# Kernel optimization log

Hardware: AMD Instinct MI355X
Metric: run time of the kernel (lower is better)

## Reference

```python
import jax, jax.numpy as jnp
import numpy as np

LAM = 0.5          # lambda_ in DyGCN
GROUPS = 4
EPS_GN = 1e-5
EPS_LN = 1e-5


def _group_norm(y, w, b):
    # y: [B, Ch, N, T]; GroupNorm over (channels-in-group, N, T)
    B, Ch, N, T = y.shape
    yr = y.reshape(B, GROUPS, Ch // GROUPS, N, T)
    mu = yr.mean(axis=(2, 3, 4), keepdims=True)
    var = yr.var(axis=(2, 3, 4), keepdims=True)
    yn = ((yr - mu) * jax.lax.rsqrt(var + EPS_GN)).reshape(B, Ch, N, T)
    return yn * w[None, :, None, None] + b[None, :, None, None]


def _gtu(X, w, b, pw, pb, qw, qb):
    # grouped conv2d, kernel (1,k), stride 1, VALID; out channels = 2*H
    xc = jax.lax.conv_general_dilated(
        X, w, window_strides=(1, 1), padding='VALID',
        feature_group_count=GROUPS,
        dimension_numbers=('NCHW', 'OIHW', 'NCHW'))
    xc = xc + b[None, :, None, None]
    H = X.shape[1]
    xp = _group_norm(xc[:, :H], pw, pb)   # matches torch chunk(2, dim=1)
    xq = _group_norm(xc[:, H:], qw, qb)
    mish = xp * jnp.tanh(jax.nn.softplus(xp))   # Mish
    gate = jnp.clip(xq, 0.0, 1.0)               # Hardtanh(0,1)
    return mish * gate


def reference(x, static_adj, U1, U2, U3, be, Ve, W0, b0, masks, Ws, bs, Wd, bd,
              conv3_w, conv5_w, conv7_w, conv9_w, conv_b,
              gn_pw, gn_pb, gn_qw, gn_qb, fc_w, fc_b, res_w, res_b, ln_w, ln_b):
    B, N, C, T = x.shape
    # ---- Temporal attention ----
    lhs = jnp.einsum('btc,cn->btn', jnp.einsum('bnct,n->btc', x, U1), U2)  # [B,T,N]
    rhs = jnp.einsum('c,bnct->bnt', U3, x)                                 # [B,N,T]
    product = jnp.einsum('btn,bns->bts', lhs, rhs)                          # [B,T,T]
    E = jnp.einsum('ij,bjk->bik', Ve, jax.nn.sigmoid(product + be))
    At = jax.nn.softmax(E, axis=1)
    x_TAt = jnp.einsum('bmt,bts->bms', x.reshape(B, N * C, T), At).reshape(B, N, C, T)
    # ---- DyGCN, vectorized across T ----
    xt = jnp.moveaxis(x_TAt, -1, 1)                                        # [B,T,N,C]
    x0 = jnp.einsum('btnc,hc->btnh', xt, W0) + b0                          # shared linear
    enh = static_adj[None] * jax.nn.sigmoid(masks)                         # [T,N,N]
    s = jnp.einsum('tnm,btmc->btnc', enh, xt)
    static_out = jnp.einsum('btnc,thc->btnh', s, Ws) + bs[None, :, None, :]
    # dynamic branch (DynamicGCNLayer): data-dependent adjacency
    scores = jnp.einsum('btnc,btmc->btnm', xt, xt) / jnp.sqrt(jnp.float32(C))
    adj = jax.nn.softmax(scores, axis=-1)                                  # [B,T,N,N]
    d = jnp.einsum('btnm,btmc->btnc', adj, xt)
    dyn_out = jnp.einsum('btnc,thc->btnh', d, Wd) + bd[None, :, None, :]
    fused = (LAM - 0.025) * static_out + (1.0 - LAM - 0.025) * dyn_out + 0.05 * x0
    X = jnp.transpose(fused, (0, 3, 2, 1))                                 # [B,H,N,T]
    # ---- multi-scale gated temporal convs ----
    outs = [
        _gtu(X, conv3_w, conv_b[0], gn_pw[0], gn_pb[0], gn_qw[0], gn_qb[0]),
        _gtu(X, conv5_w, conv_b[1], gn_pw[1], gn_pb[1], gn_qw[1], gn_qb[1]),
        _gtu(X, conv7_w, conv_b[2], gn_pw[2], gn_pb[2], gn_qw[2], gn_qb[2]),
        _gtu(X, conv9_w, conv_b[3], gn_pw[3], gn_pb[3], gn_qw[3], gn_qb[3]),
    ]
    tc = jnp.concatenate(outs, axis=-1)                                    # [B,H,N,4T-20]
    tc = jnp.einsum('bhnk,ok->bhno', tc, fc_w) + fc_b                      # fcmy (dropout=eval no-op)
    tco = jax.nn.relu(tc)                                                  # [B,H,N,T]
    # ---- residual + LayerNorm ----
    residual = jnp.einsum('bnct,hc->bhnt', x, res_w) + res_b[None, :, None, None]
    y = jax.nn.relu(residual + tco)                                        # [B,H,N,T]
    yp = jnp.transpose(y, (0, 3, 2, 1))                                    # [B,T,N,H]
    mu = yp.mean(axis=-1, keepdims=True)
    var = yp.var(axis=-1, keepdims=True)
    yn = (yp - mu) * jax.lax.rsqrt(var + EPS_LN) * ln_w + ln_b
    return jnp.transpose(yn, (0, 2, 3, 1))                                 # [B,N,H,T]


def setup_inputs():
    key = jax.random.key(0)
    ks = jax.random.split(key, 32)
    B, N, C, T, H = 16, 512, 64, 12, 64
    w = 0.05
    A = jax.random.uniform(ks[0], (N, N), jnp.float32)
    A = A / A.sum(axis=-1, keepdims=True)  # row-normalized static adjacency
    return {
        'x': jax.random.normal(ks[1], (B, N, C, T), jnp.float32),
        'static_adj': A,
        'U1': jax.random.normal(ks[2], (N,), jnp.float32) * w,
        'U2': jax.random.normal(ks[3], (C, N), jnp.float32) * w,
        'U3': jax.random.normal(ks[4], (C,), jnp.float32) * w,
        'be': jax.random.normal(ks[5], (1, T, T), jnp.float32) * w,
        'Ve': jax.random.normal(ks[6], (T, T), jnp.float32) * w,
        'W0': jax.random.normal(ks[7], (H, C), jnp.float32) * w,
        'b0': jnp.zeros((H,), jnp.float32),
        'masks': jax.random.uniform(ks[8], (T, N, N), jnp.float32, 0.8, 1.2),
        'Ws': jax.random.normal(ks[9], (T, H, C), jnp.float32) * w,
        'bs': jnp.zeros((T, H), jnp.float32),
        'Wd': jax.random.normal(ks[10], (T, H, C), jnp.float32) * w,
        'bd': jnp.zeros((T, H), jnp.float32),
        'conv3_w': jax.random.normal(ks[11], (2 * H, H // 4, 1, 3), jnp.float32) * w,
        'conv5_w': jax.random.normal(ks[12], (2 * H, H // 4, 1, 5), jnp.float32) * w,
        'conv7_w': jax.random.normal(ks[13], (2 * H, H // 4, 1, 7), jnp.float32) * w,
        'conv9_w': jax.random.normal(ks[14], (2 * H, H // 4, 1, 9), jnp.float32) * w,
        'conv_b': jnp.zeros((4, 2 * H), jnp.float32),
        'gn_pw': jnp.ones((4, H), jnp.float32),
        'gn_pb': jnp.zeros((4, H), jnp.float32),
        'gn_qw': jnp.ones((4, H), jnp.float32),
        'gn_qb': jnp.zeros((4, H), jnp.float32),
        'fc_w': jax.random.normal(ks[15], (T, 4 * T - 20), jnp.float32) * w,
        'fc_b': jnp.zeros((T,), jnp.float32),
        'res_w': jax.random.normal(ks[16], (H, C), jnp.float32) * w,
        'res_b': jnp.zeros((H,), jnp.float32),
        'ln_w': jnp.ones((H,), jnp.float32),
        'ln_b': jnp.zeros((H,), jnp.float32),
    }
```

## Files before the change

kernel.cpp:

```cpp
#include <hip/hip_runtime.h>

constexpr int Bb = 16, Nn = 512, Cc = 64, Tt = 12, Hh = 64;
constexpr int NCT = Nn * Cc * Tt;
constexpr int CT  = Cc * Tt;

__global__ void k0_rest(const float* __restrict__ rw, float* __restrict__ resT) {
    int i = blockIdx.x * 256 + threadIdx.x;
    if (i < Hh * Cc) {
        int h = i >> 6, c = i & 63;
        resT[c * 64 + h] = rw[i];
    }
}

__global__ void k1a_tmp1(const float* __restrict__ x, const float* __restrict__ U1,
                         float* __restrict__ tmp1) {
    int blk = blockIdx.x;
    int b = blk / 12; int r = blk % 12;
    int ctb = r >> 2; int nch = r & 3;
    int ct = ctb * 256 + threadIdx.x;
    const float* xb = x + (size_t)b * NCT;
    float acc = 0.f;
    int n0 = nch * 128;
    for (int n = n0; n < n0 + 128; ++n)
        acc += xb[n * CT + ct] * U1[n];
    atomicAdd(&tmp1[b * CT + ct], acc);
}

__global__ void k1b_rhs(const float* __restrict__ x, const float* __restrict__ U3,
                        float* __restrict__ rhs) {
    int wid = blockIdx.x * 4 + (threadIdx.x >> 6);
    int b = wid >> 9; int n = wid & 511;
    int l = threadIdx.x & 63;
    const float4* x4 = (const float4*)(x + (size_t)(b * Nn + n) * CT);
    float4 a0 = x4[3 * l], a1 = x4[3 * l + 1], a2 = x4[3 * l + 2];
    float xv[12] = {a0.x,a0.y,a0.z,a0.w, a1.x,a1.y,a1.z,a1.w, a2.x,a2.y,a2.z,a2.w};
    float u = U3[l];
    float p[12];
    #pragma unroll
    for (int t = 0; t < 12; ++t) p[t] = u * xv[t];
    #pragma unroll
    for (int off = 1; off < 64; off <<= 1) {
        #pragma unroll
        for (int t = 0; t < 12; ++t) p[t] += __shfl_xor(p[t], off);
    }
    if (l == 0) {
        float* rp = rhs + (size_t)(b * Nn + n) * 12;
        *(float4*)(rp)     = make_float4(p[0], p[1], p[2], p[3]);
        *(float4*)(rp + 4) = make_float4(p[4], p[5], p[6], p[7]);
        *(float4*)(rp + 8) = make_float4(p[8], p[9], p[10], p[11]);
    }
}

__global__ void k1c_att(const float* __restrict__ tmp1, const float* __restrict__ rhs,
                        const float* __restrict__ U2, const float* __restrict__ be,
                        const float* __restrict__ Ve, float* __restrict__ At) {
    __shared__ float t1[CT];
    __shared__ float rh[Nn * Tt];
    __shared__ float lh[Tt * Nn];
    __shared__ float part[576];
    __shared__ float sp[144];
    __shared__ float Ee[144];
    int b = blockIdx.x, tid = threadIdx.x;
    for (int i = tid; i < CT; i += 256) t1[i] = tmp1[b * CT + i];
    for (int i = tid; i < Nn * Tt; i += 256) rh[i] = rhs[b * Nn * Tt + i];
    __syncthreads();
    for (int nn = tid; nn < Nn; nn += 256) {
        float l[Tt];
        #pragma unroll
        for (int t = 0; t < Tt; ++t) l[t] = 0.f;
        for (int c = 0; c < Cc; ++c) {
            float u2 = U2[c * Nn + nn];
            #pragma unroll
            for (int t = 0; t < Tt; ++t) l[t] += t1[c * Tt + t] * u2;
        }
        #pragma unroll
        for (int t = 0; t < Tt; ++t) lh[t * Nn + nn] = l[t];
    }
    __syncthreads();
    for (int task = tid; task < 576; task += 256) {
        int ts = task >> 2, ch = task & 3;
        int t = ts / 12, s2 = ts % 12;
        int n0 = ch * 128;
        float a = 0.f;
        for (int nn = n0; nn < n0 + 128; ++nn) a += lh[t * Nn + nn] * rh[nn * Tt + s2];
        part[task] = a;
    }
    __syncthreads();
    if (tid < 144) {
        float a = part[tid * 4] + part[tid * 4 + 1] + part[tid * 4 + 2] + part[tid * 4 + 3]
                + be[tid];
        sp[tid] = 1.f / (1.f + __expf(-a));
    }
    __syncthreads();
    if (tid < 144) {
        int i = tid / 12, k = tid % 12;
        float a = 0.f;
        #pragma unroll
        for (int j = 0; j < 12; ++j) a += Ve[i * 12 + j] * sp[j * 12 + k];
        Ee[tid] = a;
    }
    __syncthreads();
    if (tid < 12) {
        int k = tid;
        float mx = -1e30f;
        #pragma unroll
        for (int i = 0; i < 12; ++i) mx = fmaxf(mx, Ee[i * 12 + k]);
        float su = 0.f; float ex[12];
        #pragma unroll
        for (int i = 0; i < 12; ++i) { ex[i] = __expf(Ee[i * 12 + k] - mx); su += ex[i]; }
        float inv = 1.f / su;
        #pragma unroll
        for (int i = 0; i < 12; ++i) At[b * 144 + i * 12 + k] = ex[i] * inv;
    }
}

__global__ void k2_xtt(const float* __restrict__ x, const float* __restrict__ At,
                       float* __restrict__ xtT) {
    int idx = blockIdx.x * 256 + threadIdx.x;
    int n = idx & 511; int c = (idx >> 9) & 63; int b = idx >> 15;
    const float* xr = x + (size_t)((b * Nn + n) * Cc + c) * Tt;
    float xv[Tt];
    {
        const float4* x4 = (const float4*)xr;
        float4 a0 = x4[0], a1 = x4[1], a2 = x4[2];
        xv[0]=a0.x; xv[1]=a0.y; xv[2]=a0.z; xv[3]=a0.w;
        xv[4]=a1.x; xv[5]=a1.y; xv[6]=a1.z; xv[7]=a1.w;
        xv[8]=a2.x; xv[9]=a2.y; xv[10]=a2.z; xv[11]=a2.w;
    }
    const float* Ab = At + b * 144;
    for (int t = 0; t < Tt; ++t) {
        float a = 0.f;
        #pragma unroll
        for (int u = 0; u < Tt; ++u) a += xv[u] * Ab[u * 12 + t];
        xtT[((size_t)(b * Tt + t) * Cc + c) * Nn + n] = a;
    }
}

__global__ void k2b_enh(const float* __restrict__ adj, const float* __restrict__ masks,
                        float* __restrict__ enhT) {
    __shared__ float tile[32][33];
    int blk = blockIdx.x;
    int t = blk >> 8; int r = blk & 255;
    int n0 = (r >> 4) * 32; int m0 = (r & 15) * 32;
    int tx = threadIdx.x & 31; int ty = threadIdx.x >> 5;
    #pragma unroll
    for (int i = 0; i < 4; ++i) {
        int nl = ty + 8 * i;
        float a  = adj[(n0 + nl) * Nn + m0 + tx];
        float mk = masks[t * Nn * Nn + (n0 + nl) * Nn + m0 + tx];
        tile[nl][tx] = a / (1.f + __expf(-mk));
    }
    __syncthreads();
    #pragma unroll
    for (int i = 0; i < 4; ++i) {
        int ml = ty + 8 * i;
        enhT[(size_t)(t * Nn + m0 + ml) * Nn + n0 + tx] = tile[tx][ml];
    }
}

__global__ __launch_bounds__(256, 3) void k3_gcn(
    const float* __restrict__ xtT, const float* __restrict__ enhT,
    const float* __restrict__ W0, const float* __restrict__ b0,
    const float* __restrict__ Ws, const float* __restrict__ bs,
    const float* __restrict__ Wd, const float* __restrict__ bd,
    float* __restrict__ F) {
    __shared__ float xs[64][64];
    int blk = blockIdx.x;
    int seg = blk & 7; int t = (blk >> 3) % Tt; int b = blk / (Tt * 8);
    int tid = threadIdx.x;
    int lane = tid & 63;
    int w = tid >> 6;
    int cg = lane >> 4;
    int r = lane & 15;
    int n = seg * 64 + w * 16 + r;
    int c0 = cg * 16;
    const float* xb = xtT + (size_t)(b * Tt + t) * Cc * Nn;
    float row[16], accd[16], accs[16];
    #pragma unroll
    for (int j = 0; j < 16; ++j) row[j] = xb[(c0 + j) * Nn + n];
    #pragma unroll
    for (int j = 0; j < 16; ++j) { accd[j] = 0.f; accs[j] = 0.f; }
    float sumexp = 0.f;
    const float* ehT = enhT + (size_t)t * Nn * Nn + n;
    for (int m0 = 0; m0 < Nn; m0 += 64) {
        __syncthreads();
        #pragma unroll
        for (int i = 0; i < 4; ++i) {
            int f = i * 256 + tid;
            int c = f >> 4; int mi = (f & 15) * 4;
            *(float4*)&xs[c][mi] = *(const float4*)(xb + c * Nn + m0 + mi);
        }
        __syncthreads();
        #pragma unroll 1
        for (int m4 = 0; m4 < 64; m4 += 4) {
            float e0 = ehT[(m0 + m4 + 0) * Nn];
            float e1 = ehT[(m0 + m4 + 1) * Nn];
            float e2 = ehT[(m0 + m4 + 2) * Nn];
            float e3 = ehT[(m0 + m4 + 3) * Nn];
            float4 v[16];
            #pragma unroll
            for (int j = 0; j < 16; ++j) v[j] = *(const float4*)&xs[c0 + j][m4];
            float s0 = 0.f, s1 = 0.f, s2 = 0.f, s3 = 0.f;
            #pragma unroll
            for (int j = 0; j < 16; ++j) {
                float rj = row[j];
                s0 += rj * v[j].x; s1 += rj * v[j].y;
                s2 += rj * v[j].z; s3 += rj * v[j].w;
            }
            s0 += __shfl_xor(s0, 16); s0 += __shfl_xor(s0, 32);
            s1 += __shfl_xor(s1, 16); s1 += __shfl_xor(s1, 32);
            s2 += __shfl_xor(s2, 16); s2 += __shfl_xor(s2, 32);
            s3 += __shfl_xor(s3, 16); s3 += __shfl_xor(s3, 32);
            float p0 = __expf(s0 * 0.125f), p1 = __expf(s1 * 0.125f);
            float p2 = __expf(s2 * 0.125f), p3 = __expf(s3 * 0.125f);
            sumexp += (p0 + p1) + (p2 + p3);
            #pragma unroll
            for (int j = 0; j < 16; ++j) {
                accd[j] += p0 * v[j].x + p1 * v[j].y + p2 * v[j].z + p3 * v[j].w;
                accs[j] += e0 * v[j].x + e1 * v[j].y + e2 * v[j].z + e3 * v[j].w;
            }
        }
    }
    float invd = 0.475f / sumexp;
    #pragma unroll
    for (int j = 0; j < 16; ++j) {
        accd[j] *= invd; accs[j] *= 0.475f; row[j] *= 0.05f;
    }
    const float* Wst = Ws + t * Hh * Cc;
    const float* Wdt = Wd + t * Hh * Cc;
    float* Fp = F + ((size_t)(b * Tt + t) * Nn + n) * Hh;
    for (int hb = 0; hb < 16; ++hb) {
        float oo[4];
        #pragma unroll
        for (int k = 0; k < 4; ++k) {
            int h = hb * 4 + k;
            const float4* w04 = (const float4*)(W0 + h * Cc + c0);
            const float4* ws4 = (const float4*)(Wst + h * Cc + c0);
            const float4* wd4 = (const float4*)(Wdt + h * Cc + c0);
            float a = 0.f;
            #pragma unroll
            for (int jj = 0; jj < 4; ++jj) {
                float4 wv = w04[jj], sv = ws4[jj], dv = wd4[jj];
                a += row[jj*4+0]*wv.x + row[jj*4+1]*wv.y + row[jj*4+2]*wv.z + row[jj*4+3]*wv.w;
                a += accs[jj*4+0]*sv.x + accs[jj*4+1]*sv.y + accs[jj*4+2]*sv.z + accs[jj*4+3]*sv.w;
                a += accd[jj*4+0]*dv.x + accd[jj*4+1]*dv.y + accd[jj*4+2]*dv.z + accd[jj*4+3]*dv.w;
            }
            a += __shfl_xor(a, 16);
            a += __shfl_xor(a, 32);
            oo[k] = a + 0.05f * b0[h] + 0.475f * (bs[t * Hh + h] + bd[t * Hh + h]);
        }
        if ((hb >> 2) == cg)
            *(float4*)(Fp + hb * 4) = make_float4(oo[0], oo[1], oo[2], oo[3]);
    }
}

__global__ __launch_bounds__(512) void k4_conv(
                        const float* __restrict__ F,
                        const float* __restrict__ w3, const float* __restrict__ w5,
                        const float* __restrict__ w7, const float* __restrict__ w9,
                        const float* __restrict__ cb,
                        float* __restrict__ xc, float* __restrict__ stats) {
    __shared__ float fl[4 * Tt * Hh];
    __shared__ float sstat[64];
    int blk = blockIdx.x;
    int b = blk >> 7; int n0 = (blk & 127) * 4;
    int tid = threadIdx.x;
    if (tid < 64) sstat[tid] = 0.f;
    for (int i = tid; i < 3072; i += 512) {
        int t = i >> 8; int r = i & 255;
        fl[i] = F[(size_t)(b * Tt + t) * Nn * Hh + n0 * Hh + r];
    }
    __syncthreads();
    int nl = tid >> 7; int co = tid & 127;
    int g = co >> 5;
    float a3[10], a5[8], a7[6], a9[4];
    {
        float c3 = cb[co], c5 = cb[128 + co], c7 = cb[256 + co], c9 = cb[384 + co];
        #pragma unroll
        for (int j = 0; j < 10; ++j) a3[j] = c3;
        #pragma unroll
        for (int j = 0; j < 8; ++j) a5[j] = c5;
        #pragma unroll
        for (int j = 0; j < 6; ++j) a7[j] = c7;
        #pragma unroll
        for (int j = 0; j < 4; ++j) a9[j] = c9;
    }
    for (int ci = 0; ci < 16; ++ci) {
        int cig = g * 16 + ci;
        float xr[12];
        #pragma unroll
        for (int tt = 0; tt < 12; ++tt) xr[tt] = fl[tt * 256 + nl * 64 + cig];
        const float* p3 = w3 + (co * 16 + ci) * 3;
        #pragma unroll
        for (int dt = 0; dt < 3; ++dt) {
            float wv = p3[dt];
            #pragma unroll
            for (int j = 0; j < 10; ++j) a3[j] += xr[j + dt] * wv;
        }
        const float* p5 = w5 + (co * 16 + ci) * 5;
        #pragma unroll
        for (int dt = 0; dt < 5; ++dt) {
            float wv = p5[dt];
            #pragma unroll
            for (int j = 0; j < 8; ++j) a5[j] += xr[j + dt] * wv;
        }
        const float* p7 = w7 + (co * 16 + ci) * 7;
        #pragma unroll
        for (int dt = 0; dt < 7; ++dt) {
            float wv = p7[dt];
            #pragma unroll
            for (int j = 0; j < 6; ++j) a7[j] += xr[j + dt] * wv;
        }
        const float* p9 = w9 + (co * 16 + ci) * 9;
        #pragma unroll
        for (int dt = 0; dt < 9; ++dt) {
            float wv = p9[dt];
            #pragma unroll
            for (int j = 0; j < 4; ++j) a9[j] += xr[j + dt] * wv;
        }
    }
    int pg = (co < 64) ? (co >> 4) : 4 + ((co - 64) >> 4);
    float* xcw = xc + ((size_t)(b * Nn + n0 + nl) * 128 + co) * 28;
    float su, sq;
    su = 0.f; sq = 0.f;
    #pragma unroll
    for (int j = 0; j < 10; ++j) { float v = a3[j]; xcw[j] = v; su += v; sq += v * v; }
    #pragma unroll
    for (int off = 1; off < 16; off <<= 1) { su += __shfl_xor(su, off); sq += __shfl_xor(sq, off); }
    if ((tid & 15) == 0) { atomicAdd(&sstat[(0 * 8 + pg) * 2], su); atomicAdd(&sstat[(0 * 8 + pg) * 2 + 1], sq); }
    su = 0.f; sq = 0.f;
    #pragma unroll
    for (int j = 0; j < 8; ++j) { float v = a5[j]; xcw[10 + j] = v; su += v; sq += v * v; }
    #pragma unroll
    for (int off = 1; off < 16; off <<= 1) { su += __shfl_xor(su, off); sq += __shfl_xor(sq, off); }
    if ((tid & 15) == 0) { atomicAdd(&sstat[(1 * 8 + pg) * 2], su); atomicAdd(&sstat[(1 * 8 + pg) * 2 + 1], sq); }
    su = 0.f; sq = 0.f;
    #pragma unroll
    for (int j = 0; j < 6; ++j) { float v = a7[j]; xcw[18 + j] = v; su += v; sq += v * v; }
    #pragma unroll
    for (int off = 1; off < 16; off <<= 1) { su += __shfl_xor(su, off); sq += __shfl_xor(sq, off); }
    if ((tid & 15) == 0) { atomicAdd(&sstat[(2 * 8 + pg) * 2], su); atomicAdd(&sstat[(2 * 8 + pg) * 2 + 1], sq); }
    su = 0.f; sq = 0.f;
    #pragma unroll
    for (int j = 0; j < 4; ++j) { float v = a9[j]; xcw[24 + j] = v; su += v; sq += v * v; }
    #pragma unroll
    for (int off = 1; off < 16; off <<= 1) { su += __shfl_xor(su, off); sq += __shfl_xor(sq, off); }
    if ((tid & 15) == 0) { atomicAdd(&sstat[(3 * 8 + pg) * 2], su); atomicAdd(&sstat[(3 * 8 + pg) * 2 + 1], sq); }
    __syncthreads();
    if (tid < 64) {
        int s = tid >> 4; int pgq = (tid >> 1) & 7; int st = tid & 1;
        atomicAdd(&stats[((s * Bb + b) * 8 + pgq) * 2 + st], sstat[(s * 8 + pgq) * 2 + st]);
    }
}

__global__ __launch_bounds__(256) void k5_final(
                         const float* __restrict__ xc, const float* __restrict__ stats,
                         const float* __restrict__ x,
                         const float* __restrict__ gpw, const float* __restrict__ gpb,
                         const float* __restrict__ gqw, const float* __restrict__ gqb,
                         const float* __restrict__ fcw, const float* __restrict__ fcb,
                         const float* __restrict__ resT, const float* __restrict__ rb,
                         const float* __restrict__ lnw, const float* __restrict__ lnb,
                         float* __restrict__ out) {
    int blk = blockIdx.x;
    int b = blk >> 7; int n = (blk & 127) * 4 + (threadIdx.x >> 6);
    int h = threadIdx.x & 63;
    int pg = h >> 4;
    const int TkA[4] = {10, 8, 6, 4};
    float mu_p[4], rs_p[4], mu_q[4], rs_q[4];
    #pragma unroll
    for (int s = 0; s < 4; ++s) {
        float cnt = 16.f * 512.f * (float)TkA[s];
        float su = stats[((s * Bb + b) * 8 + pg) * 2];
        float sq = stats[((s * Bb + b) * 8 + pg) * 2 + 1];
        float mu = su / cnt; float var = sq / cnt - mu * mu;
        mu_p[s] = mu; rs_p[s] = rsqrtf(var + 1e-5f);
        su = stats[((s * Bb + b) * 8 + 4 + pg) * 2];
        sq = stats[((s * Bb + b) * 8 + 4 + pg) * 2 + 1];
        mu = su / cnt; var = sq / cnt - mu * mu;
        mu_q[s] = mu; rs_q[s] = rsqrtf(var + 1e-5f);
    }
    const float* xcp = xc + ((size_t)(b * Nn + n) * 128 + h) * 28;
    const float* xcq = xcp + 64 * 28;
    float pb_[28], qb_[28];
    {
        const float4* p4 = (const float4*)xcp;
        const float4* q4 = (const float4*)xcq;
        #pragma unroll
        for (int j = 0; j < 7; ++j) {
            float4 a = p4[j];
            pb_[j*4] = a.x; pb_[j*4+1] = a.y; pb_[j*4+2] = a.z; pb_[j*4+3] = a.w;
            float4 c = q4[j];
            qb_[j*4] = c.x; qb_[j*4+1] = c.y; qb_[j*4+2] = c.z; qb_[j*4+3] = c.w;
        }
    }
    float tc[28];
    int off = 0;
    #pragma unroll
    for (int s = 0; s < 4; ++s) {
        float pw = gpw[s * 64 + h], pbv = gpb[s * 64 + h];
        float qw = gqw[s * 64 + h], qbv = gqb[s * 64 + h];
        #pragma unroll
        for (int j = 0; j < 10; ++j) {
            if (j < TkA[s]) {
                float p = (pb_[off + j] - mu_p[s]) * rs_p[s] * pw + pbv;
                float q = (qb_[off + j] - mu_q[s]) * rs_q[s] * qw + qbv;
                float mish;
                if (p > 20.f) mish = p;
                else { float z = 1.f + __expf(p); float z2 = z * z; mish = p * (z2 - 1.f) / (z2 + 1.f); }
                float gate = fminf(fmaxf(q, 0.f), 1.f);
                tc[off + j] = mish * gate;
            }
        }
        off += TkA[s];
    }
    float o[12];
    #pragma unroll
    for (int t = 0; t < 12; ++t) {
        float a = fcb[t];
        #pragma unroll
        for (int k = 0; k < 28; ++k) a += tc[k] * fcw[t * 28 + k];
        o[t] = fmaxf(a, 0.f);
    }
    const float* xr = x + (size_t)(b * Nn + n) * CT;
    float res[12];
    float rbv = rb[h];
    #pragma unroll
    for (int t = 0; t < 12; ++t) res[t] = rbv;
    for (int c = 0; c < 64; ++c) {
        float rv = resT[c * 64 + h];
        #pragma unroll
        for (int t = 0; t < 12; ++t) res[t] += xr[c * 12 + t] * rv;
    }
    float y[12];
    #pragma unroll
    for (int t = 0; t < 12; ++t) y[t] = fmaxf(res[t] + o[t], 0.f);
    float lw = lnw[h], lb = lnb[h];
    float ov[12];
    #pragma unroll
    for (int t = 0; t < 12; ++t) {
        float s1 = y[t], s2 = y[t] * y[t];
        #pragma unroll
        for (int o2 = 32; o2 > 0; o2 >>= 1) {
            s1 += __shfl_xor(s1, o2);
            s2 += __shfl_xor(s2, o2);
        }
        float mu = s1 * (1.f / 64.f);
        float var = s2 * (1.f / 64.f) - mu * mu;
        ov[t] = (y[t] - mu) * rsqrtf(var + 1e-5f) * lw + lb;
    }
    float* op = out + ((size_t)(b * Nn + n) * Hh + h) * Tt;
    *(float4*)(op)     = make_float4(ov[0], ov[1], ov[2], ov[3]);
    *(float4*)(op + 4) = make_float4(ov[4], ov[5], ov[6], ov[7]);
    *(float4*)(op + 8) = make_float4(ov[8], ov[9], ov[10], ov[11]);
}

extern "C" void kernel_launch(void* const* d_in, const int* in_sizes, int n_in,
                              void* d_out, int out_size, void* d_ws, size_t ws_size,
                              hipStream_t stream) {
    const float* x    = (const float*)d_in[0];
    const float* adj  = (const float*)d_in[1];
    const float* U1   = (const float*)d_in[2];
    const float* U2   = (const float*)d_in[3];
    const float* U3   = (const float*)d_in[4];
    const float* be   = (const float*)d_in[5];
    const float* Ve   = (const float*)d_in[6];
    const float* W0   = (const float*)d_in[7];
    const float* b0   = (const float*)d_in[8];
    const float* masks= (const float*)d_in[9];
    const float* Ws   = (const float*)d_in[10];
    const float* bs   = (const float*)d_in[11];
    const float* Wd   = (const float*)d_in[12];
    const float* bd   = (const float*)d_in[13];
    const float* w3   = (const float*)d_in[14];
    const float* w5   = (const float*)d_in[15];
    const float* w7   = (const float*)d_in[16];
    const float* w9   = (const float*)d_in[17];
    const float* cb   = (const float*)d_in[18];
    const float* gpw  = (const float*)d_in[19];
    const float* gpb  = (const float*)d_in[20];
    const float* gqw  = (const float*)d_in[21];
    const float* gqb  = (const float*)d_in[22];
    const float* fcw  = (const float*)d_in[23];
    const float* fcb  = (const float*)d_in[24];
    const float* rw   = (const float*)d_in[25];
    const float* rb   = (const float*)d_in[26];
    const float* lnw  = (const float*)d_in[27];
    const float* lnb  = (const float*)d_in[28];
    float* out = (float*)d_out;
    float* ws  = (float*)d_ws;

    float* tmp1  = ws;
    float* stats = ws + 12288;
    float* At    = ws + 13312;
    float* rhs   = ws + 15616;
    float* resT  = ws + 113920;
    float* xtT   = ws + 118016;
    float* enhT  = ws + 6409472;
    float* F     = ws + 9555200;
    float* xc    = ws + 15846656;

    hipMemsetAsync(ws, 0, 13312 * sizeof(float), stream);

    k0_rest<<<16, 256, 0, stream>>>(rw, resT);
    k1a_tmp1<<<192, 256, 0, stream>>>(x, U1, tmp1);
    k1b_rhs<<<2048, 256, 0, stream>>>(x, U3, rhs);
    k2b_enh<<<3072, 256, 0, stream>>>(adj, masks, enhT);
    k1c_att<<<16, 256, 0, stream>>>(tmp1, rhs, U2, be, Ve, At);
    k2_xtt<<<2048, 256, 0, stream>>>(x, At, xtT);
    k3_gcn<<<1536, 256, 0, stream>>>(xtT, enhT, W0, b0, Ws, bs, Wd, bd, F);
    k4_conv<<<2048, 512, 0, stream>>>(F, w3, w5, w7, w9, cb, xc, stats);
    k5_final<<<2048, 256, 0, stream>>>(xc, stats, x, gpw, gpb, gqw, gqb,
                                       fcw, fcb, resT, rb, lnw, lnb, out);
}
```

Measured before the change: 1.315 ms.

## Register-block two nodes per thread in GCN kernel and switch xt to node-major layout

Changes the intermediate xt buffer from [B,T,C,N] to [B,T,N,C] so row and tile loads become contiguous float4 copies. The GCN kernel now processes two nodes per thread, reusing each shared-memory row of xs for both, which halves the grid and halves the shared-memory traffic per FLOP. It also remaps block indices so consecutive blocks spread across (b,t) groups. The cost is four 16-wide accumulator arrays per thread, which raises register pressure under the existing launch bounds and may cause spills or lower occupancy.

```diff
diff --git a/kernel.cpp b/kernel.cpp
--- a/kernel.cpp
+++ b/kernel.cpp
@@ -115,24 +115,20 @@
 }
 
 __global__ void k2_xtt(const float* __restrict__ x, const float* __restrict__ At,
-                       float* __restrict__ xtT) {
+                       float* __restrict__ xtN) {
     int idx = blockIdx.x * 256 + threadIdx.x;
-    int n = idx & 511; int c = (idx >> 9) & 63; int b = idx >> 15;
-    const float* xr = x + (size_t)((b * Nn + n) * Cc + c) * Tt;
-    float xv[Tt];
-    {
-        const float4* x4 = (const float4*)xr;
-        float4 a0 = x4[0], a1 = x4[1], a2 = x4[2];
-        xv[0]=a0.x; xv[1]=a0.y; xv[2]=a0.z; xv[3]=a0.w;
-        xv[4]=a1.x; xv[5]=a1.y; xv[6]=a1.z; xv[7]=a1.w;
-        xv[8]=a2.x; xv[9]=a2.y; xv[10]=a2.z; xv[11]=a2.w;
-    }
+    int c = idx & 63; int n = (idx >> 6) & 511; int b = idx >> 15;
+    const float4* x4 = (const float4*)(x + (size_t)((b * Nn + n) * Cc + c) * Tt);
+    float4 a0 = x4[0], a1 = x4[1], a2 = x4[2];
+    float xv[12] = {a0.x,a0.y,a0.z,a0.w, a1.x,a1.y,a1.z,a1.w, a2.x,a2.y,a2.z,a2.w};
     const float* Ab = At + b * 144;
+    float* op = xtN + (size_t)b * Tt * Nn * Cc + n * Cc + c;
+    #pragma unroll
     for (int t = 0; t < Tt; ++t) {
         float a = 0.f;
         #pragma unroll
         for (int u = 0; u < Tt; ++u) a += xv[u] * Ab[u * 12 + t];
-        xtT[((size_t)(b * Tt + t) * Cc + c) * Nn + n] = a;
+        op[(size_t)t * Nn * Cc] = a;
     }
 }
 
@@ -159,98 +155,151 @@
 }
 
 __global__ __launch_bounds__(256, 3) void k3_gcn(
-    const float* __restrict__ xtT, const float* __restrict__ enhT,
+    const float* __restrict__ xtN, const float* __restrict__ enhT,
     const float* __restrict__ W0, const float* __restrict__ b0,
     const float* __restrict__ Ws, const float* __restrict__ bs,
     const float* __restrict__ Wd, const float* __restrict__ bd,
     float* __restrict__ F) {
     __shared__ float xs[64][64];
-    int blk = blockIdx.x;
-    int seg = blk & 7; int t = (blk >> 3) % Tt; int b = blk / (Tt * 8);
+    int blk = (blockIdx.x & 7) * 96 + (blockIdx.x >> 3);
+    int seg = blk & 3; int t = (blk >> 2) % Tt; int b = blk / (Tt * 4);
     int tid = threadIdx.x;
     int lane = tid & 63;
     int w = tid >> 6;
     int cg = lane >> 4;
     int r = lane & 15;
-    int n = seg * 64 + w * 16 + r;
+    int n0 = seg * 128 + w * 16 + r;
+    int n1 = n0 + 64;
     int c0 = cg * 16;
-    const float* xb = xtT + (size_t)(b * Tt + t) * Cc * Nn;
-    float row[16], accd[16], accs[16];
-    #pragma unroll
-    for (int j = 0; j < 16; ++j) row[j] = xb[(c0 + j) * Nn + n];
-    #pragma unroll
-    for (int j = 0; j < 16; ++j) { accd[j] = 0.f; accs[j] = 0.f; }
-    float sumexp = 0.f;
-    const float* ehT = enhT + (size_t)t * Nn * Nn + n;
+    const float* xb = xtN + (size_t)(b * Tt + t) * Nn * Cc;
+    float row0[16], row1[16];
+    {
+        const float4* r4 = (const float4*)(xb + n0 * Cc + c0);
+        const float4* s4 = (const float4*)(xb + n1 * Cc + c0);
+        #pragma unroll
+        for (int jj = 0; jj < 4; ++jj) {
+            float4 a = r4[jj];
+            row0[jj*4] = a.x; row0[jj*4+1] = a.y; row0[jj*4+2] = a.z; row0[jj*4+3] = a.w;
+            float4 bq = s4[jj];
+            row1[jj*4] = bq.x; row1[jj*4+1] = bq.y; row1[jj*4+2] = bq.z; row1[jj*4+3] = bq.w;
+        }
+    }
+    float accd0[16], accd1[16], accs0[16], accs1[16];
+    #pragma unroll
+    for (int j = 0; j < 16; ++j) { accd0[j] = 0.f; accd1[j] = 0.f; accs0[j] = 0.f; accs1[j] = 0.f; }
+    float sumexp0 = 0.f, sumexp1 = 0.f;
+    const float* eh0 = enhT + (size_t)t * Nn * Nn + n0;
+    const float* eh1 = eh0 + 64;
     for (int m0 = 0; m0 < Nn; m0 += 64) {
         __syncthreads();
-        #pragma unroll
-        for (int i = 0; i < 4; ++i) {
-            int f = i * 256 + tid;
-            int c = f >> 4; int mi = (f & 15) * 4;
-            *(float4*)&xs[c][mi] = *(const float4*)(xb + c * Nn + m0 + mi);
+        {
+            const float4* src = (const float4*)(xb + m0 * Cc);
+            float4* dst = (float4*)&xs[0][0];
+            #pragma unroll
+            for (int i = 0; i < 4; ++i) dst[i * 256 + tid] = src[i * 256 + tid];
         }
         __syncthreads();
         #pragma unroll 1
-        for (int m4 = 0; m4 < 64; m4 += 4) {
-            float e0 = ehT[(m0 + m4 + 0) * Nn];
-            float e1 = ehT[(m0 + m4 + 1) * Nn];
-            float e2 = ehT[(m0 + m4 + 2) * Nn];
-            float e3 = ehT[(m0 + m4 + 3) * Nn];
-            float4 v[16];
-            #pragma unroll
-            for (int j = 0; j < 16; ++j) v[j] = *(const float4*)&xs[c0 + j][m4];
-            float s0 = 0.f, s1 = 0.f, s2 = 0.f, s3 = 0.f;
-            #pragma unroll
-            for (int j = 0; j < 16; ++j) {
-                float rj = row[j];
-                s0 += rj * v[j].x; s1 += rj * v[j].y;
-                s2 += rj * v[j].z; s3 += rj * v[j].w;
-            }
-            s0 += __shfl_xor(s0, 16); s0 += __shfl_xor(s0, 32);
-            s1 += __shfl_xor(s1, 16); s1 += __shfl_xor(s1, 32);
-            s2 += __shfl_xor(s2, 16); s2 += __shfl_xor(s2, 32);
-            s3 += __shfl_xor(s3, 16); s3 += __shfl_xor(s3, 32);
-            float p0 = __expf(s0 * 0.125f), p1 = __expf(s1 * 0.125f);
-            float p2 = __expf(s2 * 0.125f), p3 = __expf(s3 * 0.125f);
-            sumexp += (p0 + p1) + (p2 + p3);
-            #pragma unroll
-            for (int j = 0; j < 16; ++j) {
-                accd[j] += p0 * v[j].x + p1 * v[j].y + p2 * v[j].z + p3 * v[j].w;
-                accs[j] += e0 * v[j].x + e1 * v[j].y + e2 * v[j].z + e3 * v[j].w;
-            }
-        }
-    }
-    float invd = 0.475f / sumexp;
+        for (int mm = 0; mm < 64; mm += 4) {
+            float sA[4], sB[4];
+            #pragma unroll
+            for (int k = 0; k < 4; ++k) {
+                const float4* vp = (const float4*)&xs[mm + k][c0];
+                float4 v0 = vp[0], v1 = vp[1], v2 = vp[2], v3 = vp[3];
+                float a, bq;
+                a  = row0[0]*v0.x + row0[1]*v0.y + row0[2]*v0.z + row0[3]*v0.w
+                   + row0[4]*v1.x + row0[5]*v1.y + row0[6]*v1.z + row0[7]*v1.w
+                   + row0[8]*v2.x + row0[9]*v2.y + row0[10]*v2.z + row0[11]*v2.w
+                   + row0[12]*v3.x + row0[13]*v3.y + row0[14]*v3.z + row0[15]*v3.w;
+                bq = row1[0]*v0.x + row1[1]*v0.y + row1[2]*v0.z + row1[3]*v0.w
+                   + row1[4]*v1.x + row1[5]*v1.y + row1[6]*v1.z + row1[7]*v1.w
+                   + row1[8]*v2.x + row1[9]*v2.y + row1[10]*v2.z + row1[11]*v2.w
+                   + row1[12]*v3.x + row1[13]*v3.y + row1[14]*v3.z + row1[15]*v3.w;
+                sA[k] = a; sB[k] = bq;
+            }
+            #pragma unroll
+            for (int k = 0; k < 4; ++k) {
+                sA[k] += __shfl_xor(sA[k], 16); sA[k] += __shfl_xor(sA[k], 32);
+                sB[k] += __shfl_xor(sB[k], 16); sB[k] += __shfl_xor(sB[k], 32);
+            }
+            float p[4], q[4];
+            #pragma unroll
+            for (int k = 0; k < 4; ++k) {
+                p[k] = __expf(sA[k] * 0.125f);
+                q[k] = __expf(sB[k] * 0.125f);
+            }
+            sumexp0 += (p[0] + p[1]) + (p[2] + p[3]);
+            sumexp1 += (q[0] + q[1]) + (q[2] + q[3]);
+            float e[4], f[4];
+            #pragma unroll
+            for (int k = 0; k < 4; ++k) {
+                e[k] = eh0[(size_t)(m0 + mm + k) * Nn];
+                f[k] = eh1[(size_t)(m0 + mm + k) * Nn];
+            }
+            #pragma unroll
+            for (int k = 0; k < 4; ++k) {
+                const float4* vp = (const float4*)&xs[mm + k][c0];
+                float4 v0 = vp[0], v1 = vp[1], v2 = vp[2], v3 = vp[3];
+                float pk = p[k], qk = q[k], ek = e[k], fk = f[k];
+                accd0[0]  += pk*v0.x; accd0[1]  += pk*v0.y; accd0[2]  += pk*v0.z; accd0[3]  += pk*v0.w;
+                accd0[4]  += pk*v1.x; accd0[5]  += pk*v1.y; accd0[6]  += pk*v1.z; accd0[7]  += pk*v1.w;
+                accd0[8]  += pk*v2.x; accd0[9]  += pk*v2.y; accd0[10] += pk*v2.z; accd0[11] += pk*v2.w;
+                accd0[12] += pk*v3.x; accd0[13] += pk*v3.y; accd0[14] += pk*v3.z; accd0[15] += pk*v3.w;
+                accd1[0]  += qk*v0.x; accd1[1]  += qk*v0.y; accd1[2]  += qk*v0.z; accd1[3]  += qk*v0.w;
+                accd1[4]  += qk*v1.x; accd1[5]  += qk*v1.y; accd1[6]  += qk*v1.z; accd1[7]  += qk*v1.w;
+                accd1[8]  += qk*v2.x; accd1[9]  += qk*v2.y; accd1[10] += qk*v2.z; accd1[11] += qk*v2.w;
+                accd1[12] += qk*v3.x; accd1[13] += qk*v3.y; accd1[14] += qk*v3.z; accd1[15] += qk*v3.w;
+                accs0[0]  += ek*v0.x; accs0[1]  += ek*v0.y; accs0[2]  += ek*v0.z; accs0[3]  += ek*v0.w;
+                accs0[4]  += ek*v1.x; accs0[5]  += ek*v1.y; accs0[6]  += ek*v1.z; accs0[7]  += ek*v1.w;
+                accs0[8]  += ek*v2.x; accs0[9]  += ek*v2.y; accs0[10] += ek*v2.z; accs0[11] += ek*v2.w;
+                accs0[12] += ek*v3.x; accs0[13] += ek*v3.y; accs0[14] += ek*v3.z; accs0[15] += ek*v3.w;
+                accs1[0]  += fk*v0.x; accs1[1]  += fk*v0.y; accs1[2]  += fk*v0.z; accs1[3]  += fk*v0.w;
+                accs1[4]  += fk*v1.x; accs1[5]  += fk*v1.y; accs1[6]  += fk*v1.z; accs1[7]  += fk*v1.w;
+                accs1[8]  += fk*v2.x; accs1[9]  += fk*v2.y; accs1[10] += fk*v2.z; accs1[11] += fk*v2.w;
+                accs1[12] += fk*v3.x; accs1[13] += fk*v3.y; accs1[14] += fk*v3.z; accs1[15] += fk*v3.w;
+            }
+        }
+    }
+    float invd0 = 0.475f / sumexp0;
+    float invd1 = 0.475f / sumexp1;
     #pragma unroll
     for (int j = 0; j < 16; ++j) {
-        accd[j] *= invd; accs[j] *= 0.475f; row[j] *= 0.05f;
+        accd0[j] *= invd0; accd1[j] *= invd1;
+        accs0[j] *= 0.475f; accs1[j] *= 0.475f;
+        row0[j] *= 0.05f; row1[j] *= 0.05f;
     }
     const float* Wst = Ws + t * Hh * Cc;
     const float* Wdt = Wd + t * Hh * Cc;
-    float* Fp = F + ((size_t)(b * Tt + t) * Nn + n) * Hh;
+    float* Fp0 = F + ((size_t)(b * Tt + t) * Nn + n0) * Hh;
+    float* Fp1 = F + ((size_t)(b * Tt + t) * Nn + n1) * Hh;
     for (int hb = 0; hb < 16; ++hb) {
-        float oo[4];
+        float oA[4], oB[4];
         #pragma unroll
         for (int k = 0; k < 4; ++k) {
             int h = hb * 4 + k;
             const float4* w04 = (const float4*)(W0 + h * Cc + c0);
             const float4* ws4 = (const float4*)(Wst + h * Cc + c0);
             const float4* wd4 = (const float4*)(Wdt + h * Cc + c0);
-            float a = 0.f;
+            float a = 0.f, bq = 0.f;
             #pragma unroll
             for (int jj = 0; jj < 4; ++jj) {
                 float4 wv = w04[jj], sv = ws4[jj], dv = wd4[jj];
-                a += row[jj*4+0]*wv.x + row[jj*4+1]*wv.y + row[jj*4+2]*wv.z + row[jj*4+3]*wv.w;
-                a += accs[jj*4+0]*sv.x + accs[jj*4+1]*sv.y + accs[jj*4+2]*sv.z + accs[jj*4+3]*sv.w;
-                a += accd[jj*4+0]*dv.x + accd[jj*4+1]*dv.y + accd[jj*4+2]*dv.z + accd[jj*4+3]*dv.w;
-            }
-            a += __shfl_xor(a, 16);
-            a += __shfl_xor(a, 32);
-            oo[k] = a + 0.05f * b0[h] + 0.475f * (bs[t * Hh + h] + bd[t * Hh + h]);
-        }
-        if ((hb >> 2) == cg)
-            *(float4*)(Fp + hb * 4) = make_float4(oo[0], oo[1], oo[2], oo[3]);
+                a += row0[jj*4+0]*wv.x + row0[jj*4+1]*wv.y + row0[jj*4+2]*wv.z + row0[jj*4+3]*wv.w;
+                a += accs0[jj*4+0]*sv.x + accs0[jj*4+1]*sv.y + accs0[jj*4+2]*sv.z + accs0[jj*4+3]*sv.w;
+                a += accd0[jj*4+0]*dv.x + accd0[jj*4+1]*dv.y + accd0[jj*4+2]*dv.z + accd0[jj*4+3]*dv.w;
+                bq += row1[jj*4+0]*wv.x + row1[jj*4+1]*wv.y + row1[jj*4+2]*wv.z + row1[jj*4+3]*wv.w;
+                bq += accs1[jj*4+0]*sv.x + accs1[jj*4+1]*sv.y + accs1[jj*4+2]*sv.z + accs1[jj*4+3]*sv.w;
+                bq += accd1[jj*4+0]*dv.x + accd1[jj*4+1]*dv.y + accd1[jj*4+2]*dv.z + accd1[jj*4+3]*dv.w;
+            }
+            a += __shfl_xor(a, 16);  a += __shfl_xor(a, 32);
+            bq += __shfl_xor(bq, 16); bq += __shfl_xor(bq, 32);
+            float bias = 0.05f * b0[h] + 0.475f * (bs[t * Hh + h] + bd[t * Hh + h]);
+            oA[k] = a + bias; oB[k] = bq + bias;
+        }
+        if ((hb >> 2) == cg) {
+            *(float4*)(Fp0 + hb * 4) = make_float4(oA[0], oA[1], oA[2], oA[3]);
+            *(float4*)(Fp1 + hb * 4) = make_float4(oB[0], oB[1], oB[2], oB[3]);
+        }
     }
 }
 
@@ -495,7 +544,7 @@
     float* At    = ws + 13312;
     float* rhs   = ws + 15616;
     float* resT  = ws + 113920;
-    float* xtT   = ws + 118016;
+    float* xtN   = ws + 118016;
     float* enhT  = ws + 6409472;
     float* F     = ws + 9555200;
     float* xc    = ws + 15846656;
@@ -507,8 +556,8 @@
     k1b_rhs<<<2048, 256, 0, stream>>>(x, U3, rhs);
     k2b_enh<<<3072, 256, 0, stream>>>(adj, masks, enhT);
     k1c_att<<<16, 256, 0, stream>>>(tmp1, rhs, U2, be, Ve, At);
-    k2_xtt<<<2048, 256, 0, stream>>>(x, At, xtT);
-    k3_gcn<<<1536, 256, 0, stream>>>(xtT, enhT, W0, b0, Ws, bs, Wd, bd, F);
+    k2_xtt<<<2048, 256, 0, stream>>>(x, At, xtN);
+    k3_gcn<<<768, 256, 0, stream>>>(xtN, enhT, W0, b0, Ws, bs, Wd, bd, F);
     k4_conv<<<2048, 512, 0, stream>>>(F, w3, w5, w7, w9, cb, xc, stats);
     k5_final<<<2048, 256, 0, stream>>>(xc, stats, x, gpw, gpb, gqw, gqb,
                                        fcw, fcb, resT, rb, lnw, lnb, out);
```

New measurement: 1.977 ms. +50.3%, slower.
